# Performance work log

Hardware: AMD Instinct MI355X
Metric: run time of the kernel (lower is better)

## Reference

```python
import jax, jax.numpy as jnp
import numpy as np

B, T, H, W, C = 8, 14, 64, 64, 64
F = 64  # filters (== C, so residual is identity skip)
KH, KW = 3, 3


def _hard_sigmoid(z):
    # Keras hard_sigmoid: clip(0.2*z + 0.5, 0, 1)
    return jnp.clip(0.2 * z + 0.5, 0.0, 1.0)


def _conv_same(inp, k):
    # inp: [B,H,W,Cin], k: [kh,kw,Cin,Cout]
    return jax.lax.conv_general_dilated(
        inp, k, window_strides=(1, 1), padding='SAME',
        dimension_numbers=('NHWC', 'HWIO', 'NHWC'))


def setup_inputs() -> dict:
    key = jax.random.key(0)
    k1, k2, k3, k4 = jax.random.split(key, 4)
    x = jax.random.normal(k1, (B, T, H, W, C), dtype=jnp.float32)
    Wx = jax.random.normal(k2, (KH, KW, C, 4 * F), dtype=jnp.float32) * 0.05
    Wh = jax.random.normal(k3, (KH, KW, F, 4 * F), dtype=jnp.float32) * 0.05
    b = jax.random.normal(k4, (4 * F,), dtype=jnp.float32) * 0.05
    return {'x': x, 'Wx': Wx, 'Wh': Wh, 'b': b}


def reference(x, Wx, Wh, b):
    # ConvLSTM2D (return_sequences=True) + residual add (in_ch == filters).
    # Keras gate order along channel axis: i, f, c(g), o.
    def step(carry, x_t):
        h, c = carry  # each [B,H,W,F]
        z = _conv_same(x_t, Wx) + _conv_same(h, Wh) + b  # [B,H,W,4F]
        zi, zf, zg, zo = jnp.split(z, 4, axis=-1)
        i = _hard_sigmoid(zi)
        f = _hard_sigmoid(zf)
        o = _hard_sigmoid(zo)
        c_new = f * c + i * jnp.tanh(zg)
        h_new = o * jnp.tanh(c_new)
        return (h_new, c_new), h_new

    x_t_first = jnp.moveaxis(x, 1, 0)  # [T,B,H,W,C]
    h0 = jnp.zeros((B, H, W, F), dtype=x.dtype)
    c0 = jnp.zeros((B, H, W, F), dtype=x.dtype)
    _, ys = jax.lax.scan(step, (h0, c0), x_t_first)
    y = jnp.moveaxis(ys, 0, 1)  # [B,T,H,W,F]
    return y + x  # residual skip (in_ch == filters)
```

## Files before the change

### kernel.cpp

```cpp
#include <hip/hip_runtime.h>

#define B_ 8
#define T_ 14
#define HH 64
#define WW 64
#define CC 64
#define FF 64
#define IMG (HH*WW*CC)

typedef __attribute__((ext_vector_type(8))) short short8;
typedef __attribute__((ext_vector_type(4))) float floatx4;

#define WT_OFF   0
#define C_OFF    (1u << 20)
#define H0_OFF   (C_OFF + 8u * 1024 * 1024)
#define H1_OFF   (H0_OFF + 4u * 1024 * 1024)

__device__ __forceinline__ unsigned short bf16_of(float f) {
    unsigned int x = __float_as_uint(f);
    unsigned int r = (x + 0x7FFFu + ((x >> 16) & 1u)) >> 16;
    return (unsigned short)r;
}
__device__ __forceinline__ unsigned int pack2(float a, float b) {
    return (unsigned int)bf16_of(a) | ((unsigned int)bf16_of(b) << 16);
}
__device__ __forceinline__ float hsig(float z) {
    return fminf(fmaxf(fmaf(z, 0.2f, 0.5f), 0.0f), 1.0f);
}
__device__ __forceinline__ float tanh_fast(float v) {
    float e = __expf(2.0f * v);
    return 1.0f - 2.0f / (e + 1.0f);
}

__global__ void repack_weights(const float* __restrict__ Wx,
                               const float* __restrict__ Wh,
                               unsigned short* __restrict__ Wt) {
    int u = blockIdx.x * 256 + threadIdx.x;
    int l  = u & 63;
    int nt = (u >> 6) & 15;
    int g  = (u >> 10) & 1;
    int st = u >> 11;
    const float* W = (st < 9) ? Wx : Wh;
    int tap = (st < 9) ? st : st - 9;
    int n  = nt * 16 + (l & 15);
    int c0 = g * 32 + (l >> 4) * 8;
    unsigned short tmp[8];
    #pragma unroll
    for (int j = 0; j < 8; ++j) {
        tmp[j] = bf16_of(W[(tap * 64 + c0 + j) * 256 + n]);
    }
    *(uint4*)(Wt + (size_t)u * 8) = *(const uint4*)tmp;
}

#define AT(s, r, col, c) ((((s) * 3 + (r)) * 66 + (col)) * 64 + (c))

template<bool FIRST>
__global__ __launch_bounds__(256, 2) void lstm_step_mfma(
    const float* __restrict__ x,
    const unsigned short* __restrict__ Wt,
    const float* __restrict__ bias,
    float* __restrict__ out,
    float* __restrict__ cst,
    const unsigned short* __restrict__ hprev,
    unsigned short* __restrict__ hnext,
    int t)
{
    __shared__ __align__(16) float smem[64 * 260];
    unsigned short* aT = (unsigned short*)smem;

    const int tid = threadIdx.x;
    const int l   = tid & 63;
    const int w   = tid >> 6;
    const int y   = blockIdx.x & 63;
    const int b   = blockIdx.x >> 6;
    const int m16 = l & 15;
    const int q   = l >> 4;

    const float* xbase = x + (size_t)(b * T_ + t) * IMG;

    {
        const int col = (tid >> 2) + 1;
        const int ch  = (tid & 3) * 16;
        const int sm  = (col & 7) << 3;
        #pragma unroll
        for (int r = 0; r < 3; ++r) {
            int iy = y + r - 1;
            uint4 u0 = {0, 0, 0, 0}, u1 = {0, 0, 0, 0};
            if ((unsigned)iy < (unsigned)HH) {
                const float4* s4 = (const float4*)(xbase + iy * (WW * CC)) + tid * 4;
                float4 f0 = s4[0], f1 = s4[1], f2 = s4[2], f3 = s4[3];
                u0.x = pack2(f0.x, f0.y); u0.y = pack2(f0.z, f0.w);
                u0.z = pack2(f1.x, f1.y); u0.w = pack2(f1.z, f1.w);
                u1.x = pack2(f2.x, f2.y); u1.y = pack2(f2.z, f2.w);
                u1.z = pack2(f3.x, f3.y); u1.w = pack2(f3.z, f3.w);
            }
            *(uint4*)(aT + AT(0, r, col, ch ^ sm))       = u0;
            *(uint4*)(aT + AT(0, r, col, (ch + 8) ^ sm)) = u1;
        }
        #pragma unroll
        for (int r = 0; r < 3; ++r) {
            int iy = y + r - 1;
            uint4 u0 = {0, 0, 0, 0}, u1 = {0, 0, 0, 0};
            if (!FIRST && (unsigned)iy < (unsigned)HH) {
                const uint4* hp = (const uint4*)(hprev + (size_t)(b * HH + iy) * (WW * CC));
                u0 = hp[tid * 2];
                u1 = hp[tid * 2 + 1];
            }
            *(uint4*)(aT + AT(1, r, col, ch ^ sm))       = u0;
            *(uint4*)(aT + AT(1, r, col, (ch + 8) ^ sm)) = u1;
        }
        if (tid < 96) {
            int grp = tid >> 3, l8 = tid & 7;
            int src = grp / 6, rem = grp % 6;
            int r = rem >> 1, colh = (rem & 1) * 65;
            int hm = (colh & 7) << 3;
            uint4 z = {0, 0, 0, 0};
            *(uint4*)(aT + AT(src, r, colh, (l8 * 8) ^ hm)) = z;
        }
    }
    __syncthreads();

    floatx4 acc[4][4];
    #pragma unroll
    for (int nt = 0; nt < 4; ++nt) {
        float bv = bias[w * 64 + nt * 16 + m16];
        #pragma unroll
        for (int mt = 0; mt < 4; ++mt) {
            acc[mt][nt][0] = bv; acc[mt][nt][1] = bv;
            acc[mt][nt][2] = bv; acc[mt][nt][3] = bv;
        }
    }

    const int NSRC = FIRST ? 1 : 2;
    #pragma unroll
    for (int ky = 0; ky < 3; ++ky) {
        #pragma unroll
        for (int kx = 0; kx < 3; ++kx) {
            const int swz = ((m16 + kx) & 7) << 3;
            #pragma unroll
            for (int src = 0; src < NSRC; ++src) {
                #pragma unroll
                for (int g = 0; g < 2; ++g) {
                    const int lo = (g * 32 + q * 8) ^ swz;
                    short8 af[4];
                    #pragma unroll
                    for (int mt = 0; mt < 4; ++mt) {
                        int col = mt * 16 + m16 + kx;
                        af[mt] = *(const short8*)(aT + AT(src, ky, col, lo));
                    }
                    short8 bf[4];
                    int fc = (((src * 9 + ky * 3 + kx) * 2 + g) * 16 + w * 4);
                    #pragma unroll
                    for (int nt = 0; nt < 4; ++nt) {
                        bf[nt] = *(const short8*)(Wt + (size_t)(fc + nt) * 512 + l * 8);
                    }
                    #pragma unroll
                    for (int mt = 0; mt < 4; ++mt) {
                        #pragma unroll
                        for (int nt = 0; nt < 4; ++nt) {
                            acc[mt][nt] = __builtin_amdgcn_mfma_f32_16x16x32_bf16(
                                af[mt], bf[nt], acc[mt][nt], 0, 0, 0);
                        }
                    }
                }
            }
        }
    }

    __syncthreads();
    #pragma unroll
    for (int mt = 0; mt < 4; ++mt) {
        #pragma unroll
        for (int nt = 0; nt < 4; ++nt) {
            int n = w * 64 + nt * 16 + m16;
            #pragma unroll
            for (int r = 0; r < 4; ++r) {
                int m = mt * 16 + q * 4 + r;
                smem[m * 260 + n] = acc[mt][nt][r];
            }
        }
    }
    __syncthreads();

    const int fch   = (tid & 15) * 4;
    const int mbase = tid >> 4;
    const float* xres = xbase + y * (WW * CC);
    float* outrow = out + (size_t)(b * T_ + t) * IMG + y * (WW * CC);
    #pragma unroll
    for (int i = 0; i < 4; ++i) {
        int m = mbase + i * 16;
        const float* zr = smem + m * 260;
        float4 zi = *(const float4*)(zr + fch);
        float4 zf = *(const float4*)(zr + 64 + fch);
        float4 zg = *(const float4*)(zr + 128 + fch);
        float4 zo = *(const float4*)(zr + 192 + fch);
        size_t sidx = (size_t)(b * HH + y) * (WW * CC) + m * 64 + fch;
        float4 cold = {0, 0, 0, 0};
        if (!FIRST) cold = *(const float4*)(cst + sidx);
        float4 xv = *(const float4*)(xres + m * 64 + fch);

        float cn[4], hv[4];
        float zia[4] = {zi.x, zi.y, zi.z, zi.w};
        float zfa[4] = {zf.x, zf.y, zf.z, zf.w};
        float zga[4] = {zg.x, zg.y, zg.z, zg.w};
        float zoa[4] = {zo.x, zo.y, zo.z, zo.w};
        float ca[4]  = {cold.x, cold.y, cold.z, cold.w};
        float xa[4]  = {xv.x, xv.y, xv.z, xv.w};
        #pragma unroll
        for (int k = 0; k < 4; ++k) {
            float ig = hsig(zia[k]);
            float fg = hsig(zfa[k]);
            float gg = tanh_fast(zga[k]);
            float og = hsig(zoa[k]);
            cn[k] = FIRST ? (ig * gg) : fmaf(fg, ca[k], ig * gg);
            hv[k] = og * tanh_fast(cn[k]);
        }
        float4 cnew = {cn[0], cn[1], cn[2], cn[3]};
        *(float4*)(cst + sidx) = cnew;
        ushort4 hb;
        hb.x = bf16_of(hv[0]); hb.y = bf16_of(hv[1]);
        hb.z = bf16_of(hv[2]); hb.w = bf16_of(hv[3]);
        *(ushort4*)(hnext + sidx) = hb;
        float4 yo = {hv[0] + xa[0], hv[1] + xa[1], hv[2] + xa[2], hv[3] + xa[3]};
        *(float4*)(outrow + m * 64 + fch) = yo;
    }
}

extern "C" void kernel_launch(void* const* d_in, const int* in_sizes, int n_in,
                              void* d_out, int out_size, void* d_ws, size_t ws_size,
                              hipStream_t stream) {
    const float* x    = (const float*)d_in[0];
    const float* Wx   = (const float*)d_in[1];
    const float* Wh   = (const float*)d_in[2];
    const float* bias = (const float*)d_in[3];
    float* out = (float*)d_out;

    unsigned short* Wt = (unsigned short*)((char*)d_ws + WT_OFF);
    float* cst         = (float*)((char*)d_ws + C_OFF);
    unsigned short* h0 = (unsigned short*)((char*)d_ws + H0_OFF);
    unsigned short* h1 = (unsigned short*)((char*)d_ws + H1_OFF);

    repack_weights<<<144, 256, 0, stream>>>(Wx, Wh, Wt);

    const int grid = B_ * HH;
    lstm_step_mfma<true><<<grid, 256, 0, stream>>>(x, Wt, bias, out, cst, h0, h0, 0);
    for (int t = 1; t < T_; ++t) {
        unsigned short* hp = (t & 1) ? h0 : h1;
        unsigned short* hn = (t & 1) ? h1 : h0;
        lstm_step_mfma<false><<<grid, 256, 0, stream>>>(x, Wt, bias, out, cst, hp, hn, t);
    }
}
```

Baseline: 538.8 us.

## Process two output rows per block to reuse halo rows and weight fragments

```diff
diff --git a/kernel.cpp b/kernel.cpp
--- a/kernel.cpp
+++ b/kernel.cpp
@@ -5,7 +5,6 @@
 #define HH 64
 #define WW 64
 #define CC 64
-#define FF 64
 #define IMG (HH*WW*CC)
 
 typedef __attribute__((ext_vector_type(8))) short short8;
@@ -52,7 +51,7 @@
     *(uint4*)(Wt + (size_t)u * 8) = *(const uint4*)tmp;
 }
 
-#define AT(s, r, col, c) ((((s) * 3 + (r)) * 66 + (col)) * 64 + (c))
+#define AT(s, p, col, c) ((((s) * 4 + (p)) * 66 + (col)) * 64 + (c))
 
 template<bool FIRST>
 __global__ __launch_bounds__(256, 2) void lstm_step_mfma(
@@ -65,14 +64,14 @@
     unsigned short* __restrict__ hnext,
     int t)
 {
-    __shared__ __align__(16) float smem[64 * 260];
-    unsigned short* aT = (unsigned short*)smem;
+    __shared__ __align__(16) unsigned short aT[2 * 4 * 66 * 64];
+    float* zbuf = (float*)aT;
 
     const int tid = threadIdx.x;
     const int l   = tid & 63;
     const int w   = tid >> 6;
-    const int y   = blockIdx.x & 63;
-    const int b   = blockIdx.x >> 6;
+    const int y0  = (blockIdx.x & 31) * 2;
+    const int b   = blockIdx.x >> 5;
     const int m16 = l & 15;
     const int q   = l >> 4;
 
@@ -83,8 +82,8 @@
         const int ch  = (tid & 3) * 16;
         const int sm  = (col & 7) << 3;
         #pragma unroll
-        for (int r = 0; r < 3; ++r) {
-            int iy = y + r - 1;
+        for (int r = 0; r < 4; ++r) {
+            int iy = y0 + r - 1;
             uint4 u0 = {0, 0, 0, 0}, u1 = {0, 0, 0, 0};
             if ((unsigned)iy < (unsigned)HH) {
                 const float4* s4 = (const float4*)(xbase + iy * (WW * CC)) + tid * 4;
@@ -97,37 +96,41 @@
             *(uint4*)(aT + AT(0, r, col, ch ^ sm))       = u0;
             *(uint4*)(aT + AT(0, r, col, (ch + 8) ^ sm)) = u1;
         }
-        #pragma unroll
-        for (int r = 0; r < 3; ++r) {
-            int iy = y + r - 1;
-            uint4 u0 = {0, 0, 0, 0}, u1 = {0, 0, 0, 0};
-            if (!FIRST && (unsigned)iy < (unsigned)HH) {
-                const uint4* hp = (const uint4*)(hprev + (size_t)(b * HH + iy) * (WW * CC));
-                u0 = hp[tid * 2];
-                u1 = hp[tid * 2 + 1];
-            }
-            *(uint4*)(aT + AT(1, r, col, ch ^ sm))       = u0;
-            *(uint4*)(aT + AT(1, r, col, (ch + 8) ^ sm)) = u1;
-        }
-        if (tid < 96) {
+        if (!FIRST) {
+            #pragma unroll
+            for (int r = 0; r < 4; ++r) {
+                int iy = y0 + r - 1;
+                uint4 u0 = {0, 0, 0, 0}, u1 = {0, 0, 0, 0};
+                if ((unsigned)iy < (unsigned)HH) {
+                    const uint4* hp = (const uint4*)(hprev + (size_t)(b * HH + iy) * (WW * CC));
+                    u0 = hp[tid * 2];
+                    u1 = hp[tid * 2 + 1];
+                }
+                *(uint4*)(aT + AT(1, r, col, ch ^ sm))       = u0;
+                *(uint4*)(aT + AT(1, r, col, (ch + 8) ^ sm)) = u1;
+            }
+        }
+        if (tid < 128) {
             int grp = tid >> 3, l8 = tid & 7;
-            int src = grp / 6, rem = grp % 6;
-            int r = rem >> 1, colh = (rem & 1) * 65;
+            int src = grp >> 3, rem = grp & 7;
+            int p = rem >> 1, colh = (rem & 1) * 65;
             int hm = (colh & 7) << 3;
             uint4 z = {0, 0, 0, 0};
-            *(uint4*)(aT + AT(src, r, colh, (l8 * 8) ^ hm)) = z;
+            *(uint4*)(aT + AT(src, p, colh, (l8 * 8) ^ hm)) = z;
         }
     }
     __syncthreads();
 
-    floatx4 acc[4][4];
-    #pragma unroll
-    for (int nt = 0; nt < 4; ++nt) {
-        float bv = bias[w * 64 + nt * 16 + m16];
-        #pragma unroll
-        for (int mt = 0; mt < 4; ++mt) {
-            acc[mt][nt][0] = bv; acc[mt][nt][1] = bv;
-            acc[mt][nt][2] = bv; acc[mt][nt][3] = bv;
+    float bv[4];
+    #pragma unroll
+    for (int nt = 0; nt < 4; ++nt) bv[nt] = bias[w * 64 + nt * 16 + m16];
+    floatx4 acc[8][4];
+    #pragma unroll
+    for (int mt = 0; mt < 8; ++mt) {
+        #pragma unroll
+        for (int nt = 0; nt < 4; ++nt) {
+            acc[mt][nt][0] = bv[nt]; acc[mt][nt][1] = bv[nt];
+            acc[mt][nt][2] = bv[nt]; acc[mt][nt][3] = bv[nt];
         }
     }
 
@@ -142,11 +145,12 @@
                 #pragma unroll
                 for (int g = 0; g < 2; ++g) {
                     const int lo = (g * 32 + q * 8) ^ swz;
-                    short8 af[4];
+                    short8 af[8];
                     #pragma unroll
-                    for (int mt = 0; mt < 4; ++mt) {
-                        int col = mt * 16 + m16 + kx;
-                        af[mt] = *(const short8*)(aT + AT(src, ky, col, lo));
+                    for (int mt = 0; mt < 8; ++mt) {
+                        int p    = (mt >> 2) + ky;
+                        int colr = (mt & 3) * 16 + m16 + kx;
+                        af[mt] = *(const short8*)(aT + AT(src, p, colr, lo));
                     }
                     short8 bf[4];
                     int fc = (((src * 9 + ky * 3 + kx) * 2 + g) * 16 + w * 4);
@@ -155,7 +159,7 @@
                         bf[nt] = *(const short8*)(Wt + (size_t)(fc + nt) * 512 + l * 8);
                     }
                     #pragma unroll
-                    for (int mt = 0; mt < 4; ++mt) {
+                    for (int mt = 0; mt < 8; ++mt) {
                         #pragma unroll
                         for (int nt = 0; nt < 4; ++nt) {
                             acc[mt][nt] = __builtin_amdgcn_mfma_f32_16x16x32_bf16(
@@ -167,62 +171,66 @@
         }
     }
 
-    __syncthreads();
-    #pragma unroll
-    for (int mt = 0; mt < 4; ++mt) {
-        #pragma unroll
-        for (int nt = 0; nt < 4; ++nt) {
-            int n = w * 64 + nt * 16 + m16;
-            #pragma unroll
-            for (int r = 0; r < 4; ++r) {
-                int m = mt * 16 + q * 4 + r;
-                smem[m * 260 + n] = acc[mt][nt][r];
-            }
-        }
-    }
-    __syncthreads();
-
     const int fch   = (tid & 15) * 4;
     const int mbase = tid >> 4;
-    const float* xres = xbase + y * (WW * CC);
-    float* outrow = out + (size_t)(b * T_ + t) * IMG + y * (WW * CC);
-    #pragma unroll
-    for (int i = 0; i < 4; ++i) {
-        int m = mbase + i * 16;
-        const float* zr = smem + m * 260;
-        float4 zi = *(const float4*)(zr + fch);
-        float4 zf = *(const float4*)(zr + 64 + fch);
-        float4 zg = *(const float4*)(zr + 128 + fch);
-        float4 zo = *(const float4*)(zr + 192 + fch);
-        size_t sidx = (size_t)(b * HH + y) * (WW * CC) + m * 64 + fch;
-        float4 cold = {0, 0, 0, 0};
-        if (!FIRST) cold = *(const float4*)(cst + sidx);
-        float4 xv = *(const float4*)(xres + m * 64 + fch);
-
-        float cn[4], hv[4];
-        float zia[4] = {zi.x, zi.y, zi.z, zi.w};
-        float zfa[4] = {zf.x, zf.y, zf.z, zf.w};
-        float zga[4] = {zg.x, zg.y, zg.z, zg.w};
-        float zoa[4] = {zo.x, zo.y, zo.z, zo.w};
-        float ca[4]  = {cold.x, cold.y, cold.z, cold.w};
-        float xa[4]  = {xv.x, xv.y, xv.z, xv.w};
-        #pragma unroll
-        for (int k = 0; k < 4; ++k) {
-            float ig = hsig(zia[k]);
-            float fg = hsig(zfa[k]);
-            float gg = tanh_fast(zga[k]);
-            float og = hsig(zoa[k]);
-            cn[k] = FIRST ? (ig * gg) : fmaf(fg, ca[k], ig * gg);
-            hv[k] = og * tanh_fast(cn[k]);
-        }
-        float4 cnew = {cn[0], cn[1], cn[2], cn[3]};
-        *(float4*)(cst + sidx) = cnew;
-        ushort4 hb;
-        hb.x = bf16_of(hv[0]); hb.y = bf16_of(hv[1]);
-        hb.z = bf16_of(hv[2]); hb.w = bf16_of(hv[3]);
-        *(ushort4*)(hnext + sidx) = hb;
-        float4 yo = {hv[0] + xa[0], hv[1] + xa[1], hv[2] + xa[2], hv[3] + xa[3]};
-        *(float4*)(outrow + m * 64 + fch) = yo;
+    #pragma unroll
+    for (int hf = 0; hf < 2; ++hf) {
+        __syncthreads();
+        #pragma unroll
+        for (int mt4 = 0; mt4 < 4; ++mt4) {
+            #pragma unroll
+            for (int nt = 0; nt < 4; ++nt) {
+                int n = w * 64 + nt * 16 + m16;
+                #pragma unroll
+                for (int r = 0; r < 4; ++r) {
+                    int m = mt4 * 16 + q * 4 + r;
+                    zbuf[m * 260 + n] = acc[hf * 4 + mt4][nt][r];
+                }
+            }
+        }
+        __syncthreads();
+
+        const int yo = y0 + hf;
+        const float* xres = xbase + yo * (WW * CC);
+        float* outrow = out + (size_t)(b * T_ + t) * IMG + yo * (WW * CC);
+        #pragma unroll
+        for (int i = 0; i < 4; ++i) {
+            int m = mbase + i * 16;
+            const float* zr = zbuf + m * 260;
+            float4 zi = *(const float4*)(zr + fch);
+            float4 zf = *(const float4*)(zr + 64 + fch);
+            float4 zg = *(const float4*)(zr + 128 + fch);
+            float4 zo = *(const float4*)(zr + 192 + fch);
+            size_t sidx = (size_t)(b * HH + yo) * (WW * CC) + m * 64 + fch;
+            float4 cold = {0, 0, 0, 0};
+            if (!FIRST) cold = *(const float4*)(cst + sidx);
+            float4 xv = *(const float4*)(xres + m * 64 + fch);
+
+            float cn[4], hv[4];
+            float zia[4] = {zi.x, zi.y, zi.z, zi.w};
+            float zfa[4] = {zf.x, zf.y, zf.z, zf.w};
+            float zga[4] = {zg.x, zg.y, zg.z, zg.w};
+            float zoa[4] = {zo.x, zo.y, zo.z, zo.w};
+            float ca[4]  = {cold.x, cold.y, cold.z, cold.w};
+            float xa[4]  = {xv.x, xv.y, xv.z, xv.w};
+            #pragma unroll
+            for (int k = 0; k < 4; ++k) {
+                float ig = hsig(zia[k]);
+                float fg = hsig(zfa[k]);
+                float gg = tanh_fast(zga[k]);
+                float og = hsig(zoa[k]);
+                cn[k] = FIRST ? (ig * gg) : fmaf(fg, ca[k], ig * gg);
+                hv[k] = og * tanh_fast(cn[k]);
+            }
+            float4 cnew = {cn[0], cn[1], cn[2], cn[3]};
+            *(float4*)(cst + sidx) = cnew;
+            ushort4 hb;
+            hb.x = bf16_of(hv[0]); hb.y = bf16_of(hv[1]);
+            hb.z = bf16_of(hv[2]); hb.w = bf16_of(hv[3]);
+            *(ushort4*)(hnext + sidx) = hb;
+            float4 yv = {hv[0] + xa[0], hv[1] + xa[1], hv[2] + xa[2], hv[3] + xa[3]};
+            *(float4*)(outrow + m * 64 + fch) = yv;
+        }
     }
 }
 
@@ -242,7 +250,7 @@
 
     repack_weights<<<144, 256, 0, stream>>>(Wx, Wh, Wt);
 
-    const int grid = B_ * HH;
+    const int grid = B_ * (HH / 2);
     lstm_step_mfma<true><<<grid, 256, 0, stream>>>(x, Wt, bias, out, cst, h0, h0, 0);
     for (int t = 1; t < T_; ++t) {
         unsigned short* hp = (t & 1) ? h0 : h1;
```

Result: slower. 964.0 us (+78.9%).
